# Optimization experiments

Hardware: AMD Instinct MI355X
Metric: run time of the kernel (lower is better)

Reference implementation:

```python
import jax, jax.numpy as jnp
import numpy as np


def setup_inputs() -> dict:
    key = jax.random.key(0)
    k_h, k_src, k_dst, k_w = jax.random.split(key, 4)
    N, F, E, OUT = 100000, 128, 640000, 16
    h = jax.random.normal(k_h, (N, F), dtype=jnp.float32)
    src = jax.random.randint(k_src, (E,), 0, N, dtype=jnp.int64)
    dst = jax.random.randint(k_dst, (E,), 0, N, dtype=jnp.int64)
    # Linear(2F, OUT): weight [OUT, 2F], bias [OUT]
    W = jax.random.normal(k_w, (OUT, 2 * F), dtype=jnp.float32) / np.sqrt(2.0 * F)
    b = jnp.zeros((OUT,), dtype=jnp.float32)
    return {"h": h, "src": src, "dst": dst, "W": W, "b": b}


def reference(h, src, dst, W, b):
    # Per-edge gather of source/dest node features, concat, linear.
    # Dropout is identity in eval mode (p=0.2 during training only).
    h_u = h[src]                      # [E, F]
    h_v = h[dst]                      # [E, F]
    F_dim = h.shape[1]
    W_u, W_v = W[:, :F_dim], W[:, F_dim:]
    # Equivalent to concat([h_u, h_v], -1) @ W.T + b, without materializing concat
    score = jnp.einsum('ef,of->eo', h_u, W_u) + jnp.einsum('ef,of->eo', h_v, W_v) + b
    return score
```

## Files before the change

### kernel.cpp

```cpp
#include <hip/hip_runtime.h>
#include <hip/hip_bf16.h>

#define F_DIM 128
#define OUT_DIM 16

typedef _Float16 half8 __attribute__((ext_vector_type(8)));
typedef float floatx4 __attribute__((ext_vector_type(4)));
typedef unsigned short us8 __attribute__((ext_vector_type(8)));

__global__ __launch_bounds__(256) void wprep_kernel(
    const float* __restrict__ W, _Float16* __restrict__ Bhi,
    _Float16* __restrict__ Blo)
{
    int tid = blockIdx.x * 256 + threadIdx.x;
    if (tid >= 4096) return;
    int j    = tid & 7;
    int lane = (tid >> 3) & 63;
    int t    = (tid >> 9) & 1;
    int s    = (tid >> 10) & 3;
    int n = lane & 15;
    int q = lane >> 4;
    int k = s * 32 + q * 8 + j;
    float w = W[n * 256 + t * 128 + k];
    _Float16 hi = (_Float16)w;
    _Float16 lo = (_Float16)(w - (float)hi);
    Bhi[tid] = hi;
    Blo[tid] = lo;
}

__device__ __forceinline__ unsigned bf16_bits_rne(float f) {
    unsigned u = __builtin_bit_cast(unsigned, f);
    unsigned rounding = 0x7FFFu + ((u >> 16) & 1u);
    return (u + rounding) >> 16;
}

__global__ __launch_bounds__(256) void proj_mfma_kernel(
    const float* __restrict__ h, const _Float16* __restrict__ Bhi,
    const _Float16* __restrict__ Blo, const float* __restrict__ b,
    unsigned int* __restrict__ Pu16, unsigned int* __restrict__ Pv16, int N)
{
    const int lane = threadIdx.x & 63;
    const int wave = threadIdx.x >> 6;
    const int n = lane & 15;
    const int q = lane >> 4;
    const int row_base = blockIdx.x * 64 + wave * 16;
    if (row_base >= N) return;

    int arow = row_base + n;
    if (arow >= N) arow = N - 1;
    const float* hrow = h + (size_t)arow * F_DIM + q * 8;

    floatx4 c0 = {0.f, 0.f, 0.f, 0.f};
    floatx4 c1 = {0.f, 0.f, 0.f, 0.f};

    #pragma unroll
    for (int s = 0; s < 4; ++s) {
        float av[8];
        *(float4*)(av)     = *(const float4*)(hrow + s * 32);
        *(float4*)(av + 4) = *(const float4*)(hrow + s * 32 + 4);
        half8 ah, al;
        #pragma unroll
        for (int j = 0; j < 8; ++j) {
            _Float16 hi = (_Float16)av[j];
            ah[j] = hi;
            al[j] = (_Float16)(av[j] - (float)hi);
        }
        const int base0 = (s * 2 + 0) * 512 + lane * 8;
        const int base1 = (s * 2 + 1) * 512 + lane * 8;
        half8 wh0 = *(const half8*)(Bhi + base0);
        half8 wl0 = *(const half8*)(Blo + base0);
        half8 wh1 = *(const half8*)(Bhi + base1);
        half8 wl1 = *(const half8*)(Blo + base1);

        c0 = __builtin_amdgcn_mfma_f32_16x16x32_f16(wh0, ah, c0, 0, 0, 0);
        c0 = __builtin_amdgcn_mfma_f32_16x16x32_f16(wl0, ah, c0, 0, 0, 0);
        c0 = __builtin_amdgcn_mfma_f32_16x16x32_f16(wh0, al, c0, 0, 0, 0);
        c1 = __builtin_amdgcn_mfma_f32_16x16x32_f16(wh1, ah, c1, 0, 0, 0);
        c1 = __builtin_amdgcn_mfma_f32_16x16x32_f16(wl1, ah, c1, 0, 0, 0);
        c1 = __builtin_amdgcn_mfma_f32_16x16x32_f16(wh1, al, c1, 0, 0, 0);
    }

    const int node = row_base + n;
    if (node < N) {
        const floatx4 bv = *(const floatx4*)(b + 4 * q);
        unsigned u0 = bf16_bits_rne(c0[0] + bv[0]) | (bf16_bits_rne(c0[1] + bv[1]) << 16);
        unsigned u1 = bf16_bits_rne(c0[2] + bv[2]) | (bf16_bits_rne(c0[3] + bv[3]) << 16);
        unsigned v0 = bf16_bits_rne(c1[0]) | (bf16_bits_rne(c1[1]) << 16);
        unsigned v1 = bf16_bits_rne(c1[2]) | (bf16_bits_rne(c1[3]) << 16);
        const size_t base = (size_t)node * 8 + 2 * q;
        Pu16[base]     = u0;
        Pu16[base + 1] = u1;
        Pv16[base]     = v0;
        Pv16[base + 1] = v1;
    }
}

__global__ __launch_bounds__(256) void gather_kernel(
    const unsigned short* __restrict__ Pu, const unsigned short* __restrict__ Pv,
    const int* __restrict__ src, const int* __restrict__ dst,
    float* __restrict__ out, int E)
{
    const int tid = blockIdx.x * blockDim.x + threadIdx.x;
    const int e = tid >> 1;
    const int q = tid & 1;
    if (e >= E) return;
    const int s = src[e];
    const int d = dst[e];
    const us8 pu = *(const us8*)(Pu + (size_t)s * 16 + q * 8);
    const us8 pv = *(const us8*)(Pv + (size_t)d * 16 + q * 8);
    floatx4 r0, r1;
    #pragma unroll
    for (int j = 0; j < 4; ++j) {
        r0[j] = __uint_as_float((unsigned)pu[j] << 16)
              + __uint_as_float((unsigned)pv[j] << 16);
        r1[j] = __uint_as_float((unsigned)pu[j + 4] << 16)
              + __uint_as_float((unsigned)pv[j + 4] << 16);
    }
    floatx4* o = (floatx4*)out + (size_t)tid * 2;
    __builtin_nontemporal_store(r0, o);
    __builtin_nontemporal_store(r1, o + 1);
}

__global__ __launch_bounds__(256) void direct_kernel(
    const float* __restrict__ h, const int* __restrict__ src,
    const int* __restrict__ dst, const float* __restrict__ W,
    const float* __restrict__ b, float* __restrict__ out, int E)
{
    const int tid = blockIdx.x * blockDim.x + threadIdx.x;
    if (tid >= E * OUT_DIM) return;
    const int e = tid >> 4;
    const int o = tid & 15;
    const float* hu = h + (size_t)src[e] * F_DIM;
    const float* hv = h + (size_t)dst[e] * F_DIM;
    const float* wu = W + (size_t)o * 256;
    const float* wv = wu + 128;
    float acc = b[o];
    for (int k = 0; k < 128; ++k) acc = fmaf(hu[k], wu[k], acc);
    for (int k = 0; k < 128; ++k) acc = fmaf(hv[k], wv[k], acc);
    out[tid] = acc;
}

extern "C" void kernel_launch(void* const* d_in, const int* in_sizes, int n_in,
                              void* d_out, int out_size, void* d_ws, size_t ws_size,
                              hipStream_t stream) {
    const float* h   = (const float*)d_in[0];
    const int*   src = (const int*)d_in[1];
    const int*   dst = (const int*)d_in[2];
    const float* W   = (const float*)d_in[3];
    const float* b   = (const float*)d_in[4];
    float* out = (float*)d_out;

    const int N = in_sizes[0] / F_DIM;
    const int E = in_sizes[1];

    const size_t p16_bytes = (size_t)N * 8 * sizeof(unsigned);
    const size_t p16_al    = (p16_bytes + 255) & ~(size_t)255;
    const size_t bf_bytes  = 4096 * sizeof(_Float16);

    if (ws_size >= 2 * p16_al + 2 * bf_bytes) {
        unsigned int* Pu16 = (unsigned int*)d_ws;
        unsigned int* Pv16 = (unsigned int*)((char*)d_ws + p16_al);
        _Float16*     Bhi  = (_Float16*)((char*)d_ws + 2 * p16_al);
        _Float16*     Blo  = Bhi + 4096;

        wprep_kernel<<<16, 256, 0, stream>>>(W, Bhi, Blo);

        const int blocks1 = (N + 63) / 64;
        proj_mfma_kernel<<<blocks1, 256, 0, stream>>>(h, Bhi, Blo, b, Pu16, Pv16, N);

        const int total2  = E * 2;
        const int blocks2 = (total2 + 255) / 256;
        gather_kernel<<<blocks2, 256, 0, stream>>>(
            (const unsigned short*)Pu16, (const unsigned short*)Pv16,
            src, dst, out, E);
    } else {
        const int total  = E * OUT_DIM;
        const int blocks = (total + 255) / 256;
        direct_kernel<<<blocks, 256, 0, stream>>>(h, src, dst, W, b, out, E);
    }
}
```

Baseline: 125.9 us.

## Fuse weight prep, projection and gather into one cooperative persistent kernel

Replaces the three-kernel sequence (weight split, MFMA node projection, edge gather) with a single cooperative kernel. Each block builds the hi/lo fp16 weight tiles in shared memory, grid-strides over node tiles, then waits on a grid-wide sync before grid-striding over the edge gather. The aim is to remove two kernel launches and their inter-kernel gaps. In exchange it adds a grid barrier, a grid capped at 2048 blocks, redundant weight prep in every block, and a fallback to the old path if the cooperative launch fails.

```diff
diff --git a/kernel.cpp b/kernel.cpp
--- a/kernel.cpp
+++ b/kernel.cpp
@@ -1,12 +1,133 @@
 #include <hip/hip_runtime.h>
 #include <hip/hip_bf16.h>
+#include <hip/hip_cooperative_groups.h>
 
 #define F_DIM 128
 #define OUT_DIM 16
+
+namespace cg = cooperative_groups;
 
 typedef _Float16 half8 __attribute__((ext_vector_type(8)));
 typedef float floatx4 __attribute__((ext_vector_type(4)));
 typedef unsigned short us8 __attribute__((ext_vector_type(8)));
+
+__device__ __forceinline__ unsigned bf16_bits_rne(float f) {
+    unsigned u = __builtin_bit_cast(unsigned, f);
+    unsigned rounding = 0x7FFFu + ((u >> 16) & 1u);
+    return (u + rounding) >> 16;
+}
+
+__global__ __launch_bounds__(256) void fused_kernel(
+    const float* __restrict__ h, const int* __restrict__ src,
+    const int* __restrict__ dst, const float* __restrict__ W,
+    const float* __restrict__ b, float* __restrict__ out,
+    unsigned int* __restrict__ Pu16, unsigned int* __restrict__ Pv16,
+    int N, int E)
+{
+    __shared__ __align__(16) _Float16 sBhi[4096];
+    __shared__ __align__(16) _Float16 sBlo[4096];
+    for (int i = threadIdx.x; i < 4096; i += 256) {
+        int j    = i & 7;
+        int ln   = (i >> 3) & 63;
+        int t    = (i >> 9) & 1;
+        int s    = (i >> 10) & 3;
+        int n2 = ln & 15;
+        int q2 = ln >> 4;
+        int k = s * 32 + q2 * 8 + j;
+        float w = W[n2 * 256 + t * 128 + k];
+        _Float16 hi = (_Float16)w;
+        sBhi[i] = hi;
+        sBlo[i] = (_Float16)(w - (float)hi);
+    }
+    __syncthreads();
+
+    const int lane = threadIdx.x & 63;
+    const int wave = threadIdx.x >> 6;
+    const int n = lane & 15;
+    const int q = lane >> 4;
+    const floatx4 bv = *(const floatx4*)(b + 4 * q);
+
+    const int nTiles = (N + 15) >> 4;
+    const int waveId = blockIdx.x * 4 + wave;
+    const int nWaves = gridDim.x * 4;
+    for (int tile = waveId; tile < nTiles; tile += nWaves) {
+        const int row_base = tile * 16;
+        int arow = row_base + n;
+        if (arow >= N) arow = N - 1;
+        const float* hrow = h + (size_t)arow * F_DIM + q * 8;
+
+        floatx4 c0 = {0.f, 0.f, 0.f, 0.f};
+        floatx4 c1 = {0.f, 0.f, 0.f, 0.f};
+
+        #pragma unroll
+        for (int s = 0; s < 4; ++s) {
+            float av[8];
+            *(floatx4*)(av)     = *(const floatx4*)(hrow + s * 32);
+            *(floatx4*)(av + 4) = *(const floatx4*)(hrow + s * 32 + 4);
+            half8 ah, al;
+            #pragma unroll
+            for (int j = 0; j < 8; ++j) {
+                _Float16 hi = (_Float16)av[j];
+                ah[j] = hi;
+                al[j] = (_Float16)(av[j] - (float)hi);
+            }
+            const int base0 = (s * 2 + 0) * 512 + lane * 8;
+            const int base1 = (s * 2 + 1) * 512 + lane * 8;
+            half8 wh0 = *(const half8*)(sBhi + base0);
+            half8 wl0 = *(const half8*)(sBlo + base0);
+            half8 wh1 = *(const half8*)(sBhi + base1);
+            half8 wl1 = *(const half8*)(sBlo + base1);
+
+            c0 = __builtin_amdgcn_mfma_f32_16x16x32_f16(wh0, ah, c0, 0, 0, 0);
+            c0 = __builtin_amdgcn_mfma_f32_16x16x32_f16(wl0, ah, c0, 0, 0, 0);
+            c0 = __builtin_amdgcn_mfma_f32_16x16x32_f16(wh0, al, c0, 0, 0, 0);
+            c1 = __builtin_amdgcn_mfma_f32_16x16x32_f16(wh1, ah, c1, 0, 0, 0);
+            c1 = __builtin_amdgcn_mfma_f32_16x16x32_f16(wl1, ah, c1, 0, 0, 0);
+            c1 = __builtin_amdgcn_mfma_f32_16x16x32_f16(wh1, al, c1, 0, 0, 0);
+        }
+
+        const int node = row_base + n;
+        if (node < N) {
+            unsigned u0 = bf16_bits_rne(c0[0] + bv[0]) | (bf16_bits_rne(c0[1] + bv[1]) << 16);
+            unsigned u1 = bf16_bits_rne(c0[2] + bv[2]) | (bf16_bits_rne(c0[3] + bv[3]) << 16);
+            unsigned v0 = bf16_bits_rne(c1[0]) | (bf16_bits_rne(c1[1]) << 16);
+            unsigned v1 = bf16_bits_rne(c1[2]) | (bf16_bits_rne(c1[3]) << 16);
+            const size_t base = (size_t)node * 8 + 2 * q;
+            Pu16[base]     = u0;
+            Pu16[base + 1] = u1;
+            Pv16[base]     = v0;
+            Pv16[base + 1] = v1;
+        }
+    }
+
+    __threadfence();
+    cg::this_grid().sync();
+
+    const unsigned short* Pu = (const unsigned short*)Pu16;
+    const unsigned short* Pv = (const unsigned short*)Pv16;
+    const int tid0   = blockIdx.x * 256 + threadIdx.x;
+    const int stride = gridDim.x * 256;
+    const int total  = 2 * E;
+    for (int t = tid0; t < total; t += stride) {
+        const int e  = t >> 1;
+        const int qq = t & 1;
+        const int si = src[e];
+        const int di = dst[e];
+        const us8 pu = *(const us8*)(Pu + (size_t)si * 16 + qq * 8);
+        const us8 pv = *(const us8*)(Pv + (size_t)di * 16 + qq * 8);
+        floatx4 r0, r1;
+        #pragma unroll
+        for (int j = 0; j < 4; ++j) {
+            r0[j] = __uint_as_float((unsigned)pu[j] << 16)
+                  + __uint_as_float((unsigned)pv[j] << 16);
+            r1[j] = __uint_as_float((unsigned)pu[j + 4] << 16)
+                  + __uint_as_float((unsigned)pv[j + 4] << 16);
+        }
+        floatx4* o = (floatx4*)out + (size_t)t * 2;
+        __builtin_nontemporal_store(r0, o);
+        __builtin_nontemporal_store(r1, o + 1);
+    }
+}
 
 __global__ __launch_bounds__(256) void wprep_kernel(
     const float* __restrict__ W, _Float16* __restrict__ Bhi,
@@ -28,12 +149,6 @@
     Blo[tid] = lo;
 }
 
-__device__ __forceinline__ unsigned bf16_bits_rne(float f) {
-    unsigned u = __builtin_bit_cast(unsigned, f);
-    unsigned rounding = 0x7FFFu + ((u >> 16) & 1u);
-    return (u + rounding) >> 16;
-}
-
 __global__ __launch_bounds__(256) void proj_mfma_kernel(
     const float* __restrict__ h, const _Float16* __restrict__ Bhi,
     const _Float16* __restrict__ Blo, const float* __restrict__ b,
@@ -56,8 +171,8 @@
     #pragma unroll
     for (int s = 0; s < 4; ++s) {
         float av[8];
-        *(float4*)(av)     = *(const float4*)(hrow + s * 32);
-        *(float4*)(av + 4) = *(const float4*)(hrow + s * 32 + 4);
+        *(floatx4*)(av)     = *(const floatx4*)(hrow + s * 32);
+        *(floatx4*)(av + 4) = *(const floatx4*)(hrow + s * 32 + 4);
         half8 ah, al;
         #pragma unroll
         for (int j = 0; j < 8; ++j) {
@@ -150,32 +265,59 @@
     const float* b   = (const float*)d_in[4];
     float* out = (float*)d_out;
 
-    const int N = in_sizes[0] / F_DIM;
-    const int E = in_sizes[1];
+    int N = in_sizes[0] / F_DIM;
+    int E = in_sizes[1];
 
     const size_t p16_bytes = (size_t)N * 8 * sizeof(unsigned);
     const size_t p16_al    = (p16_bytes + 255) & ~(size_t)255;
     const size_t bf_bytes  = 4096 * sizeof(_Float16);
 
-    if (ws_size >= 2 * p16_al + 2 * bf_bytes) {
-        unsigned int* Pu16 = (unsigned int*)d_ws;
-        unsigned int* Pv16 = (unsigned int*)((char*)d_ws + p16_al);
-        _Float16*     Bhi  = (_Float16*)((char*)d_ws + 2 * p16_al);
-        _Float16*     Blo  = Bhi + 4096;
-
-        wprep_kernel<<<16, 256, 0, stream>>>(W, Bhi, Blo);
-
-        const int blocks1 = (N + 63) / 64;
-        proj_mfma_kernel<<<blocks1, 256, 0, stream>>>(h, Bhi, Blo, b, Pu16, Pv16, N);
-
-        const int total2  = E * 2;
-        const int blocks2 = (total2 + 255) / 256;
-        gather_kernel<<<blocks2, 256, 0, stream>>>(
-            (const unsigned short*)Pu16, (const unsigned short*)Pv16,
-            src, dst, out, E);
-    } else {
+    if (ws_size < 2 * p16_al + 2 * bf_bytes) {
         const int total  = E * OUT_DIM;
         const int blocks = (total + 255) / 256;
         direct_kernel<<<blocks, 256, 0, stream>>>(h, src, dst, W, b, out, E);
-    }
-}
+        return;
+    }
+
+    unsigned int* Pu16 = (unsigned int*)d_ws;
+    unsigned int* Pv16 = (unsigned int*)((char*)d_ws + p16_al);
+    _Float16*     Bhi  = (_Float16*)((char*)d_ws + 2 * p16_al);
+    _Float16*     Blo  = Bhi + 4096;
+
+    static int s_grid = -2;
+    if (s_grid == -2) {
+        int nBlk = 0;
+        if (hipOccupancyMaxActiveBlocksPerMultiprocessor(
+                &nBlk, fused_kernel, 256, 0) != hipSuccess || nBlk <= 0) {
+            s_grid = -1;
+        } else {
+            int dev = 0, nCU = 0;
+            hipGetDevice(&dev);
+            if (hipDeviceGetAttribute(&nCU, hipDeviceAttributeMultiprocessorCount,
+                                      dev) != hipSuccess || nCU <= 0)
+                nCU = 256;
+            long g = (long)nBlk * (long)nCU;
+            if (g > 2048) g = 2048;
+            s_grid = (int)g;
+        }
+    }
+
+    if (s_grid > 0) {
+        void* args[] = { (void*)&h, (void*)&src, (void*)&dst, (void*)&W,
+                         (void*)&b, (void*)&out, (void*)&Pu16, (void*)&Pv16,
+                         (void*)&N, (void*)&E };
+        hipError_t err = hipLaunchCooperativeKernel(
+            (const void*)fused_kernel, dim3(s_grid), dim3(256), args, 0, stream);
+        if (err == hipSuccess) return;
+        s_grid = -1;
+    }
+
+    wprep_kernel<<<16, 256, 0, stream>>>(W, Bhi, Blo);
+    const int blocks1 = (N + 63) / 64;
+    proj_mfma_kernel<<<blocks1, 256, 0, stream>>>(h, Bhi, Blo, b, Pu16, Pv16, N);
+    const int total2  = E * 2;
+    const int blocks2 = (total2 + 255) / 256;
+    gather_kernel<<<blocks2, 256, 0, stream>>>(
+        (const unsigned short*)Pu16, (const unsigned short*)Pv16,
+        src, dst, out, E);
+}
```

New measurement: 232.6 us. 84.8% more time.
